# Kernel optimization log

Measured on AMD Instinct MI355X. Metric: run time of the kernel, lower is better.

## Reference

```python
import jax, jax.numpy as jnp
import numpy as np

T, H, E, I, K = 2048, 2048, 32, 768, 8  # tokens, hidden, experts, moe_intermediate, top_k


def setup_inputs() -> dict:
    key = jax.random.key(0)
    k1, k2, k3, k4, k5 = jax.random.split(key, 5)
    return {
        "hidden_states": jax.random.normal(k1, (T, H), dtype=jnp.float32),
        "w_gate": jax.random.normal(k2, (H, E), dtype=jnp.float32) * 0.02,
        "w_gate_proj": jax.random.normal(k3, (E, H, I), dtype=jnp.float32) * 0.02,
        "w_up_proj": jax.random.normal(k4, (E, H, I), dtype=jnp.float32) * 0.02,
        "w_down_proj": jax.random.normal(k5, (E, I, H), dtype=jnp.float32) * 0.02,
    }


def reference(hidden_states, w_gate, w_gate_proj, w_up_proj, w_down_proj):
    # Router: softmax over expert logits, top-k, renormalize (RoutingMethodType.Renormalize,
    # norm_topk_prob=True in Qwen3 MoE config).
    x = hidden_states                                  # [T, H]
    n_tok = x.shape[0]
    logits = x @ w_gate                                # [T, E]
    probs = jax.nn.softmax(logits, axis=-1)            # [T, E]
    topk_w, topk_idx = jax.lax.top_k(probs, K)         # [T, K]
    topk_w = topk_w / jnp.sum(topk_w, axis=-1, keepdims=True)
    # Sparse combine weights [T, E]: zero except the K selected experts per token.
    combine = jnp.zeros_like(probs).at[jnp.arange(n_tok)[:, None], topk_idx].set(topk_w)

    # Expert SwiGLU MLPs (gate/up/down), computed for all experts then combined with
    # the sparse weights -- mathematically identical to top-k dispatch + grouped GEMM.
    g = jnp.einsum('th,ehi->tei', x, w_gate_proj)      # [T, E, I]
    u = jnp.einsum('th,ehi->tei', x, w_up_proj)        # [T, E, I]
    act = jax.nn.silu(g) * u                           # [T, E, I]
    # Combine expert outputs without materializing [T, E, H].
    out = jnp.einsum('tei,eih,te->th', act, w_down_proj, combine)  # [T, H]
    return out
```

## Files before the change

kernel.cpp:

```cpp
#include <hip/hip_runtime.h>

#define T_TOK 2048
#define HD    2048
#define NE    32
#define ID    768
#define TOPK  8
#define NPAIR (T_TOK * TOPK)
#define MAXT  160

typedef short bf16x8 __attribute__((ext_vector_type(8)));
typedef float f32x4  __attribute__((ext_vector_type(4)));

__device__ inline unsigned short f2bf(float f) {
    unsigned u = __builtin_bit_cast(unsigned, f);
    u += 0x7FFF + ((u >> 16) & 1);
    return (unsigned short)(u >> 16);
}

__device__ inline void gload16(const void* g, void* l) {
    __builtin_amdgcn_global_load_lds(
        (const __attribute__((address_space(1))) unsigned*)g,
        (__attribute__((address_space(3))) unsigned*)l, 16, 0, 0);
}


#define NT_GU2 3072
#define NT_D2  3072
#define NB_CVT 2048
#define NB_RTR 2048

__device__ inline void transpose_strip(const float* __restrict__ src, unsigned short* __restrict__ dst,
                                       int R, int C, int r0, int c0, char* lds) {
    int tid = threadIdx.x;
    int w = tid >> 6, l = tid & 63;
    #pragma unroll
    for (int q = 0; q < 16; ++q) {
        int s = w * 16 + q;
        const float* gp = src + (size_t)(r0 + s) * C + c0 + ((l ^ ((s >> 3) & 7)) << 2);
        gload16(gp, lds + s * 1024);
    }
    __syncthreads();
    #pragma unroll
    for (int jj = 0; jj < 8; ++jj) {
        int idx = tid + 256 * jj;
        int c = idx >> 3, tt = idx & 7;
        const char* base = lds + tt * 8192 + ((((c >> 2) ^ tt) << 4) | ((c & 3) << 2));
        unsigned short o[8];
        #pragma unroll
        for (int j = 0; j < 8; ++j)
            o[j] = f2bf(*(const float*)(base + j * 1024));
        uint4 v;
        unsigned* pv = (unsigned*)&v;
        pv[0] = (unsigned)o[0] | ((unsigned)o[1] << 16);
        pv[1] = (unsigned)o[2] | ((unsigned)o[3] << 16);
        pv[2] = (unsigned)o[4] | ((unsigned)o[5] << 16);
        pv[3] = (unsigned)o[6] | ((unsigned)o[7] << 16);
        *(uint4*)&dst[(size_t)(c0 + c) * R + r0 + 8 * tt] = v;
    }
}

__global__ __launch_bounds__(256)
void prep_all(const float* __restrict__ x, const float* __restrict__ wg,
              const float* __restrict__ wgp, const float* __restrict__ wup,
              const float* __restrict__ wdp,
              unsigned short* __restrict__ X16,
              unsigned short* __restrict__ WG, unsigned short* __restrict__ WU,
              unsigned short* __restrict__ WD,
              int* __restrict__ topk_idx, float* __restrict__ topk_w,
              int* __restrict__ counts) {
    __shared__ __align__(16) char lds[65536];
    int bid = blockIdx.x;

    if (bid < NT_GU2) {
        int e = bid / 96, ti = bid % 96;
        int r0 = (ti & 31) * 64, c0 = (ti >> 5) * 256;
        transpose_strip(wgp + (size_t)e * HD * ID, WG + (size_t)e * HD * ID, HD, ID, r0, c0, lds);
        return;
    }
    bid -= NT_GU2;
    if (bid < NT_GU2) {
        int e = bid / 96, ti = bid % 96;
        int r0 = (ti & 31) * 64, c0 = (ti >> 5) * 256;
        transpose_strip(wup + (size_t)e * HD * ID, WU + (size_t)e * HD * ID, HD, ID, r0, c0, lds);
        return;
    }
    bid -= NT_GU2;
    if (bid < NT_D2) {
        int e = bid / 96, ti = bid % 96;
        int r0 = (ti % 12) * 64, c0 = (ti / 12) * 256;
        transpose_strip(wdp + (size_t)e * ID * HD, WD + (size_t)e * ID * HD, ID, HD, r0, c0, lds);
        return;
    }
    bid -= NT_D2;
    if (bid < NB_CVT) {
        int i = bid * 256 + threadIdx.x;
        const float4* src = (const float4*)x + (size_t)i * 2;
        float4 a = src[0], b = src[1];
        uint4 r;
        r.x = (unsigned)f2bf(a.x) | ((unsigned)f2bf(a.y) << 16);
        r.y = (unsigned)f2bf(a.z) | ((unsigned)f2bf(a.w) << 16);
        r.z = (unsigned)f2bf(b.x) | ((unsigned)f2bf(b.y) << 16);
        r.w = (unsigned)f2bf(b.z) | ((unsigned)f2bf(b.w) << 16);
        *(uint4*)(X16 + (size_t)i * 8) = r;
        return;
    }
    bid -= NB_CVT;
    {
        int t = bid;
        int tid = threadIdx.x;
        int e = tid & 31, seg = tid >> 5;
        const float* xr = x + (size_t)t * HD + seg * 256;
        const float* wp = wg + (size_t)(seg * 256) * NE + e;
        float acc = 0.f;
        #pragma unroll 4
        for (int j = 0; j < 256; ++j) acc += xr[j] * wp[j * NE];
        float* part = (float*)lds;
        float* lg = part + 8 * 33;
        part[seg * 33 + e] = acc;
        __syncthreads();
        if (tid < 32) {
            float s = 0.f;
            #pragma unroll
            for (int g = 0; g < 8; ++g) s += part[g * 33 + tid];
            lg[tid] = s;
        }
        __syncthreads();
        if (tid == 0) {
            float m = lg[0];
            for (int i = 1; i < 32; ++i) m = fmaxf(m, lg[i]);
            for (int i = 0; i < 32; ++i) lg[i] = __expf(lg[i] - m);
            int   idxs[TOPK]; float wv[TOPK]; float wsum = 0.f;
            #pragma unroll
            for (int k = 0; k < TOPK; ++k) {
                float best = -1.f; int bi = 0;
                for (int i = 0; i < 32; ++i) if (lg[i] > best) { best = lg[i]; bi = i; }
                idxs[k] = bi; wv[k] = best; wsum += best; lg[bi] = -1.f;
            }
            #pragma unroll
            for (int k = 0; k < TOPK; ++k) {
                topk_idx[t * TOPK + k] = idxs[k];
                topk_w[t * TOPK + k]   = wv[k] / wsum;
                atomicAdd(&counts[idxs[k]], 1);
            }
        }
    }
}

__global__ void build_tiles(const int* __restrict__ counts, int* __restrict__ cursor,
                            int* __restrict__ tE, int* __restrict__ tStart,
                            int* __restrict__ tCnt) {
    if (threadIdx.x == 0 && blockIdx.x == 0) {
        int run = 0, nt = 0;
        for (int e = 0; e < NE; ++e) {
            cursor[e] = run;
            int c = counts[e];
            int nte = (c + 127) >> 7;
            for (int j = 0; j < nte; ++j) {
                tE[nt] = e;
                tStart[nt] = run + j * 128;
                tCnt[nt] = (c - j * 128 < 128) ? (c - j * 128) : 128;
                ++nt;
            }
            run += nte * 128;
        }
        for (; nt < MAXT; ++nt) { tE[nt] = -1; tStart[nt] = 0; tCnt[nt] = 0; }
    }
}

__global__ void scatter_kernel(const int* __restrict__ topk_idx, int* __restrict__ cursor,
                               int* __restrict__ token_list) {
    int i = blockIdx.x * 256 + threadIdx.x;
    int e = topk_idx[i];
    int pos = atomicAdd(&cursor[e], 1);
    token_list[pos] = i;
}

__global__ __launch_bounds__(256, 2)
void gemm1_kernel(const unsigned short* __restrict__ X16,
                  const unsigned short* __restrict__ WG, const unsigned short* __restrict__ WU,
                  const int* __restrict__ token_list,
                  const int* __restrict__ tE, const int* __restrict__ tStart,
                  const int* __restrict__ tCnt, unsigned short* __restrict__ act16) {
    int tile = blockIdx.x / 6, it = blockIdx.x % 6;
    int e = tE[tile];
    if (e < 0) return;
    int start = tStart[tile], cnt = tCnt[tile];
    int i0 = it * 128;

    __shared__ __align__(16) unsigned short As[128 * 64];
    __shared__ __align__(16) unsigned short Bg[128 * 64];
    __shared__ __align__(16) unsigned short Bu[128 * 64];
    __shared__ int rowTok[128];

    int tid = threadIdx.x;
    if (tid < 128)
        rowTok[tid] = (tid < cnt) ? (token_list[start + tid] >> 3) : 0;
    __syncthreads();

    int lane = tid & 63, w = tid >> 6;
    int sub = lane & 7, lrow = lane >> 3;

    const unsigned short* aP[4]; const unsigned short* gP[4]; const unsigned short* uP[4];
    #pragma unroll
    for (int c = 0; c < 4; ++c) {
        int q = w * 4 + c;
        int r = q * 8 + lrow;
        int chunk = (sub ^ (r & 7)) * 8;
        aP[c] = X16 + (size_t)rowTok[r] * HD + chunk;
        gP[c] = WG + ((size_t)e * ID + i0 + r) * HD + chunk;
        uP[c] = WU + ((size_t)e * ID + i0 + r) * HD + chunk;
    }

    f32x4 accg[4][4], accu[4][4];
    #pragma unroll
    for (int m = 0; m < 4; ++m)
        #pragma unroll
        for (int n = 0; n < 4; ++n) {
            f32x4 z = {0.f, 0.f, 0.f, 0.f};
            accg[m][n] = z; accu[m][n] = z;
        }

    int wm = w >> 1, wn = w & 1, l15 = lane & 15, lhi = lane >> 4;
    const bf16x8* Af = (const bf16x8*)As;
    const bf16x8* Gf = (const bf16x8*)Bg;
    const bf16x8* Uf = (const bf16x8*)Bu;

    for (int k0 = 0; k0 < HD; k0 += 64) {
        #pragma unroll
        for (int c = 0; c < 4; ++c) {
            int q = w * 4 + c;
            gload16(aP[c] + k0, (char*)As + q * 1024);
            gload16(gP[c] + k0, (char*)Bg + q * 1024);
            gload16(uP[c] + k0, (char*)Bu + q * 1024);
        }
        __syncthreads();
        #pragma unroll
        for (int ks = 0; ks < 2; ++ks) {
            int cc = ks * 4 + lhi;
            bf16x8 a[4], bg[4], bu[4];
            #pragma unroll
            for (int m = 0; m < 4; ++m) { int r = wm * 64 + m * 16 + l15; a[m] = Af[r * 8 + (cc ^ (r & 7))]; }
            #pragma unroll
            for (int n = 0; n < 4; ++n) {
                int r = wn * 64 + n * 16 + l15;
                bg[n] = Gf[r * 8 + (cc ^ (r & 7))];
                bu[n] = Uf[r * 8 + (cc ^ (r & 7))];
            }
            #pragma unroll
            for (int m = 0; m < 4; ++m)
                #pragma unroll
                for (int n = 0; n < 4; ++n) {
                    accg[m][n] = __builtin_amdgcn_mfma_f32_16x16x32_bf16(a[m], bg[n], accg[m][n], 0, 0, 0);
                    accu[m][n] = __builtin_amdgcn_mfma_f32_16x16x32_bf16(a[m], bu[n], accu[m][n], 0, 0, 0);
                }
        }
        __syncthreads();
    }

    #pragma unroll
    for (int m = 0; m < 4; ++m) {
        int rb = wm * 64 + m * 16 + lhi * 4;
        #pragma unroll
        for (int q = 0; q < 4; ++q) {
            int r = rb + q;
            size_t orow = (size_t)(start + r) * ID + i0 + wn * 64;
            #pragma unroll
            for (int n = 0; n < 4; ++n) {
                float g = accg[m][n][q], uu = accu[m][n][q];
                float a = g / (1.f + __expf(-g)) * uu;
                act16[orow + n * 16 + l15] = f2bf(a);
            }
        }
    }
}

__global__ __launch_bounds__(256, 2)
void gemm2_kernel(const unsigned short* __restrict__ act16, const unsigned short* __restrict__ WD,
                  const int* __restrict__ token_list,
                  const int* __restrict__ tE, const int* __restrict__ tStart,
                  const int* __restrict__ tCnt, const float* __restrict__ topk_w,
                  float* __restrict__ out) {
    int tile = blockIdx.x / 8, ht = blockIdx.x % 8;
    int e = tE[tile];
    if (e < 0) return;
    int start = tStart[tile], cnt = tCnt[tile];
    int h0 = ht * 256;

    __shared__ __align__(16) unsigned short As[128 * 64];
    __shared__ __align__(16) unsigned short Bs[256 * 64];
    __shared__ int   rowTok[128];
    __shared__ float rowW[128];

    int tid = threadIdx.x;
    if (tid < 128) {
        if (tid < cnt) { int v = token_list[start + tid]; rowTok[tid] = v >> 3; rowW[tid] = topk_w[v]; }
        else           { rowTok[tid] = 0;                 rowW[tid] = 0.f; }
    }
    __syncthreads();

    int lane = tid & 63, w = tid >> 6;
    int sub = lane & 7, lrow = lane >> 3;

    const unsigned short* aP[4]; const unsigned short* bP[8];
    #pragma unroll
    for (int c = 0; c < 4; ++c) {
        int q = w * 4 + c;
        int r = q * 8 + lrow;
        int chunk = (sub ^ (r & 7)) * 8;
        aP[c] = act16 + (size_t)(start + r) * ID + chunk;
    }
    #pragma unroll
    for (int c = 0; c < 8; ++c) {
        int q = w * 8 + c;
        int r = q * 8 + lrow;
        int chunk = (sub ^ (r & 7)) * 8;
        bP[c] = WD + ((size_t)e * HD + h0 + r) * ID + chunk;
    }

    f32x4 acc[4][8];
    #pragma unroll
    for (int m = 0; m < 4; ++m)
        #pragma unroll
        for (int n = 0; n < 8; ++n) { f32x4 z = {0.f, 0.f, 0.f, 0.f}; acc[m][n] = z; }

    int wm = w >> 1, wn = w & 1, l15 = lane & 15, lhi = lane >> 4;
    const bf16x8* Af = (const bf16x8*)As;
    const bf16x8* Bf = (const bf16x8*)Bs;

    for (int k0 = 0; k0 < ID; k0 += 64) {
        #pragma unroll
        for (int c = 0; c < 4; ++c) {
            int q = w * 4 + c;
            gload16(aP[c] + k0, (char*)As + q * 1024);
        }
        #pragma unroll
        for (int c = 0; c < 8; ++c) {
            int q = w * 8 + c;
            gload16(bP[c] + k0, (char*)Bs + q * 1024);
        }
        __syncthreads();
        #pragma unroll
        for (int ks = 0; ks < 2; ++ks) {
            int cc = ks * 4 + lhi;
            bf16x8 a[4], b[8];
            #pragma unroll
            for (int m = 0; m < 4; ++m) { int r = wm * 64 + m * 16 + l15; a[m] = Af[r * 8 + (cc ^ (r & 7))]; }
            #pragma unroll
            for (int n = 0; n < 8; ++n) { int r = wn * 128 + n * 16 + l15; b[n] = Bf[r * 8 + (cc ^ (r & 7))]; }
            #pragma unroll
            for (int m = 0; m < 4; ++m)
                #pragma unroll
                for (int n = 0; n < 8; ++n)
                    acc[m][n] = __builtin_amdgcn_mfma_f32_16x16x32_bf16(a[m], b[n], acc[m][n], 0, 0, 0);
        }
        __syncthreads();
    }

    #pragma unroll
    for (int m = 0; m < 4; ++m) {
        int rb = wm * 64 + m * 16 + lhi * 4;
        #pragma unroll
        for (int q = 0; q < 4; ++q) {
            int r = rb + q;
            if (r < cnt) {
                int tok = rowTok[r];
                float wgt = rowW[r];
                float* orow = out + (size_t)tok * HD + h0 + wn * 128;
                #pragma unroll
                for (int n = 0; n < 8; ++n)
                    atomicAdd(&orow[n * 16 + l15], acc[m][n][q] * wgt);
            }
        }
    }
}

extern "C" void kernel_launch(void* const* d_in, const int* in_sizes, int n_in,
                              void* d_out, int out_size, void* d_ws, size_t ws_size,
                              hipStream_t stream) {
    const float* x   = (const float*)d_in[0];
    const float* wg  = (const float*)d_in[1];
    const float* wgp = (const float*)d_in[2];
    const float* wup = (const float*)d_in[3];
    const float* wdp = (const float*)d_in[4];
    float* out = (float*)d_out;

    char* ws = (char*)d_ws;
    size_t off = 0;
    unsigned short* X16   = (unsigned short*)(ws + off); off += (size_t)T_TOK * HD * 2;
    unsigned short* act16 = (unsigned short*)(ws + off); off += (size_t)MAXT * 128 * ID * 2;
    int*   topk_idx   = (int*)(ws + off);   off += NPAIR * 4;
    float* topk_w     = (float*)(ws + off); off += NPAIR * 4;
    int*   token_list = (int*)(ws + off);   off += MAXT * 128 * 4;
    int*   counts     = (int*)(ws + off);   off += 256;
    int*   cursor     = (int*)(ws + off);   off += 256;
    int*   tE         = (int*)(ws + off);   off += MAXT * 4;
    int*   tStart     = (int*)(ws + off);   off += MAXT * 4;
    int*   tCnt       = (int*)(ws + off);   off += MAXT * 4;
    off = (off + 255) & ~(size_t)255;
    unsigned short* WG = (unsigned short*)(ws + off); off += (size_t)NE * ID * HD * 2;
    unsigned short* WU = (unsigned short*)(ws + off); off += (size_t)NE * ID * HD * 2;
    unsigned short* WD = (unsigned short*)(ws + off); off += (size_t)NE * HD * ID * 2;
    (void)in_sizes; (void)n_in; (void)out_size; (void)ws_size;

    hipMemsetAsync(counts, 0, 256, stream);
    hipMemsetAsync(d_out, 0, (size_t)T_TOK * HD * 4, stream);

    prep_all<<<NT_GU2 + NT_GU2 + NT_D2 + NB_CVT + NB_RTR, 256, 0, stream>>>(
        x, wg, wgp, wup, wdp, X16, WG, WU, WD, topk_idx, topk_w, counts);

    build_tiles<<<1, 64, 0, stream>>>(counts, cursor, tE, tStart, tCnt);
    scatter_kernel<<<NPAIR / 256, 256, 0, stream>>>(topk_idx, cursor, token_list);

    gemm1_kernel<<<MAXT * 6, 256, 0, stream>>>(X16, WG, WU, token_list, tE, tStart, tCnt, act16);
    gemm2_kernel<<<MAXT * 8, 256, 0, stream>>>(act16, WD, token_list, tE, tStart, tCnt, topk_w, out);
}
```

Baseline: 642.1 us.

## Store transposed bf16 expert weights in tiled blocks for contiguous GEMM loads

The prep kernel now writes each transposed bf16 weight strip as a contiguous 256x64 block instead of scattering rows across the full row-major matrix. The gate/up and down GEMM kernels compute addresses in this blocked layout, so each K-step loads one contiguous 32KB tile. The aim is fully sequential global writes in the transpose and contiguous, TLB-friendly weight loads in the GEMMs. It relies on the GEMM tile shapes matching the block layout exactly, for example h0 being derived from ht.

```diff
diff --git a/kernel.cpp b/kernel.cpp
--- a/kernel.cpp
+++ b/kernel.cpp
@@ -29,8 +29,8 @@
 #define NB_CVT 2048
 #define NB_RTR 2048
 
-__device__ inline void transpose_strip(const float* __restrict__ src, unsigned short* __restrict__ dst,
-                                       int R, int C, int r0, int c0, char* lds) {
+__device__ inline void transpose_strip(const float* __restrict__ src, unsigned short* __restrict__ dstr,
+                                       int C, int r0, int c0, char* lds) {
     int tid = threadIdx.x;
     int w = tid >> 6, l = tid & 63;
     #pragma unroll
@@ -55,7 +55,7 @@
         pv[1] = (unsigned)o[2] | ((unsigned)o[3] << 16);
         pv[2] = (unsigned)o[4] | ((unsigned)o[5] << 16);
         pv[3] = (unsigned)o[6] | ((unsigned)o[7] << 16);
-        *(uint4*)&dst[(size_t)(c0 + c) * R + r0 + 8 * tt] = v;
+        *(uint4*)&dstr[(size_t)idx * 8] = v;
     }
 }
 
@@ -74,21 +74,27 @@
     if (bid < NT_GU2) {
         int e = bid / 96, ti = bid % 96;
         int r0 = (ti & 31) * 64, c0 = (ti >> 5) * 256;
-        transpose_strip(wgp + (size_t)e * HD * ID, WG + (size_t)e * HD * ID, HD, ID, r0, c0, lds);
+        unsigned short* dstr = WG + (size_t)e * HD * ID
+                             + ((size_t)(c0 >> 8) * 32 + (r0 >> 6)) * 16384;
+        transpose_strip(wgp + (size_t)e * HD * ID, dstr, ID, r0, c0, lds);
         return;
     }
     bid -= NT_GU2;
     if (bid < NT_GU2) {
         int e = bid / 96, ti = bid % 96;
         int r0 = (ti & 31) * 64, c0 = (ti >> 5) * 256;
-        transpose_strip(wup + (size_t)e * HD * ID, WU + (size_t)e * HD * ID, HD, ID, r0, c0, lds);
+        unsigned short* dstr = WU + (size_t)e * HD * ID
+                             + ((size_t)(c0 >> 8) * 32 + (r0 >> 6)) * 16384;
+        transpose_strip(wup + (size_t)e * HD * ID, dstr, ID, r0, c0, lds);
         return;
     }
     bid -= NT_GU2;
     if (bid < NT_D2) {
         int e = bid / 96, ti = bid % 96;
         int r0 = (ti % 12) * 64, c0 = (ti / 12) * 256;
-        transpose_strip(wdp + (size_t)e * ID * HD, WD + (size_t)e * ID * HD, ID, HD, r0, c0, lds);
+        unsigned short* dstr = WD + (size_t)e * ID * HD
+                             + ((size_t)(c0 >> 8) * 12 + (r0 >> 6)) * 16384;
+        transpose_strip(wdp + (size_t)e * ID * HD, dstr, HD, r0, c0, lds);
         return;
     }
     bid -= NT_D2;
@@ -207,8 +213,10 @@
         int r = q * 8 + lrow;
         int chunk = (sub ^ (r & 7)) * 8;
         aP[c] = X16 + (size_t)rowTok[r] * HD + chunk;
-        gP[c] = WG + ((size_t)e * ID + i0 + r) * HD + chunk;
-        uP[c] = WU + ((size_t)e * ID + i0 + r) * HD + chunk;
+        int i = i0 + r;
+        size_t bbase = ((size_t)((i >> 8) * 32) * 256 + (i & 255)) * 64 + chunk;
+        gP[c] = WG + (size_t)e * ID * HD + bbase;
+        uP[c] = WU + (size_t)e * ID * HD + bbase;
     }
 
     f32x4 accg[4][4], accu[4][4];
@@ -230,8 +238,8 @@
         for (int c = 0; c < 4; ++c) {
             int q = w * 4 + c;
             gload16(aP[c] + k0, (char*)As + q * 1024);
-            gload16(gP[c] + k0, (char*)Bg + q * 1024);
-            gload16(uP[c] + k0, (char*)Bu + q * 1024);
+            gload16(gP[c] + (size_t)k0 * 256, (char*)Bg + q * 1024);
+            gload16(uP[c] + (size_t)k0 * 256, (char*)Bu + q * 1024);
         }
         __syncthreads();
         #pragma unroll
@@ -314,7 +322,7 @@
         int q = w * 8 + c;
         int r = q * 8 + lrow;
         int chunk = (sub ^ (r & 7)) * 8;
-        bP[c] = WD + ((size_t)e * HD + h0 + r) * ID + chunk;
+        bP[c] = WD + (size_t)e * HD * ID + ((size_t)(ht * 12) * 256 + r) * 64 + chunk;
     }
 
     f32x4 acc[4][8];
@@ -336,7 +344,7 @@
         #pragma unroll
         for (int c = 0; c < 8; ++c) {
             int q = w * 8 + c;
-            gload16(bP[c] + k0, (char*)Bs + q * 1024);
+            gload16(bP[c] + (size_t)k0 * 256, (char*)Bs + q * 1024);
         }
         __syncthreads();
         #pragma unroll
```

Result: no change. 636.1 us (-0.9%).
